# Kernel optimization log

Measured on AMD Instinct MI355X. Metric: run time of the kernel, lower is better.

Reference implementation:

```python
import jax, jax.numpy as jnp
import numpy as np

B, C, D, H, W = 4, 64, 16, 16, 16
C8 = C // 8


def setup_inputs() -> dict:
    key = jax.random.key(0)
    ks = jax.random.split(key, 9)
    s = lambda k, sh: jax.random.normal(k, sh, dtype=jnp.float32)
    return {
        "x_source": s(ks[0], (B, C, D, H, W)),
        "x_target": s(ks[1], (B, C, D, H, W)),
        "Wq": s(ks[2], (C8, C)) * 0.05,
        "bq": s(ks[3], (C8,)) * 0.05,
        "Wk": s(ks[4], (C8, C)) * 0.05,
        "bk": s(ks[5], (C8,)) * 0.05,
        "Wv": s(ks[6], (C, C)) * 0.05,
        "bv": s(ks[7], (C,)) * 0.05,
        "gamma": s(ks[8], (1,)) * 0.1,
    }


def reference(x_source, x_target, Wq, bq, Wk, bk, Wv, bv, gamma):
    b, c, d, h, w = x_source.shape
    n = d * h * w
    xs = x_source.reshape(b, c, n)   # (B, C, N)
    xt = x_target.reshape(b, c, n)
    # 1x1x1 convs == per-token linear projections
    q = jnp.einsum("oc,bcn->bno", Wq, xt) + bq[None, None, :]   # (B, N, C8)
    k = jnp.einsum("oc,bcn->bon", Wk, xs) + bk[None, :, None]   # (B, C8, N)
    v = jnp.einsum("oc,bcn->bon", Wv, xs) + bv[None, :, None]   # (B, C, N)
    # unscaled single-head full attention over all N = D*H*W tokens
    attn = jax.nn.softmax(jnp.einsum("bno,bom->bnm", q, k), axis=-1)  # (B, N, N)
    out = jnp.einsum("bcm,bnm->bcn", v, attn)                   # (B, C, N)
    out = out.reshape(b, c, d, h, w)
    return gamma * out + x_target
```

## Files before the change

### kernel.cpp

```cpp
#include <hip/hip_runtime.h>
#include <hip/hip_bf16.h>


typedef __attribute__((ext_vector_type(8)))  short s16x8;
typedef __attribute__((ext_vector_type(16))) float f32x16;

constexpr int B  = 4;
constexpr int C  = 64;
constexpr int N  = 4096;
constexpr int CH = 32;
constexpr int NC = 32;

__device__ __forceinline__ ushort f2bf(float x) {
    union { __hip_bfloat16 h; ushort u; } cv;
    cv.h = __float2bfloat16(x);
    return cv.u;
}
__device__ __forceinline__ uint pk2(float a, float b) {
    union { __hip_bfloat162 h2; uint u; } cv;
    cv.h2.x = __float2bfloat16(a);
    cv.h2.y = __float2bfloat16(b);
    return cv.u;
}
__device__ __forceinline__ float exp2_fast(float x) {
#if __has_builtin(__builtin_amdgcn_exp2f)
    return __builtin_amdgcn_exp2f(x);
#else
    float e;
    asm("v_exp_f32 %0, %1" : "=v"(e) : "v"(x));
    return e;
#endif
}

__global__ __launch_bounds__(320) void proj_kernel(
    const float* __restrict__ xs, const float* __restrict__ xt,
    const float* __restrict__ Wq, const float* __restrict__ bq,
    const float* __restrict__ Wk, const float* __restrict__ bk,
    const float* __restrict__ Wv, const float* __restrict__ bv,
    ushort* __restrict__ qg, ushort* __restrict__ kg, ushort* __restrict__ vf)
{
    __shared__ float sWv[64 * 64];
    __shared__ float sWk[8 * 64];
    __shared__ float sWq[8 * 64];
    __shared__ float sB[80];

    const int tid = threadIdx.x;
    for (int i = tid; i < 4096; i += 320) sWv[i] = Wv[i];
    for (int i = tid; i < 512;  i += 320) { sWk[i] = Wk[i]; sWq[i] = Wq[i]; }
    if (tid < 64)                sB[tid] = bv[tid];
    else if (tid < 72)           sB[tid] = bk[tid - 64];
    else if (tid < 80)           sB[tid] = bq[tid - 72];
    __syncthreads();

    const int grp = tid >> 5;
    const int tok = tid & 31;
    const int b   = blockIdx.x >> 7;
    const int n   = ((blockIdx.x & 127) << 5) + tok;

    const float* Wsel; const float* bsel; const float* xsel;
    if (grp < 8)       { Wsel = sWv + grp * 8 * C; bsel = sB + grp * 8; xsel = xs; }
    else if (grp == 8) { Wsel = sWk;               bsel = sB + 64;      xsel = xs; }
    else               { Wsel = sWq;               bsel = sB + 72;      xsel = xt; }

    float acc[8];
#pragma unroll
    for (int j = 0; j < 8; j++) acc[j] = bsel[j];

    const float* xcol = xsel + (size_t)b * C * N + n;
#pragma unroll 2
    for (int ci = 0; ci < C; ci += 4) {
        float x0 = xcol[(size_t)(ci + 0) * N];
        float x1 = xcol[(size_t)(ci + 1) * N];
        float x2 = xcol[(size_t)(ci + 2) * N];
        float x3 = xcol[(size_t)(ci + 3) * N];
#pragma unroll
        for (int j = 0; j < 8; j++) {
            const float4 w4 = *(const float4*)&Wsel[j * C + ci];
            acc[j] += w4.x * x0 + w4.y * x1 + w4.z * x2 + w4.w * x3;
        }
    }

    if (grp < 8) {
        const int c   = n >> 5;
        const int kk  = n & 31;
        const int ks  = kk >> 4;
        const int Gd  = (kk >> 3) & 1;
        const int j   = kk & 7;
        const int f   = grp >> 2;
        const int cb  = (grp & 3) * 8;
        ushort* base = vf + ((size_t)(b * 128 + c) * 2048) + ks * 1024 + f * 512 + j;
#pragma unroll
        for (int jc = 0; jc < 8; jc++)
            base[(size_t)(Gd * 32 + cb + jc) * 8] = f2bf(acc[jc]);
    } else {
        if (grp == 9) {
#pragma unroll
            for (int j = 0; j < 8; j++) acc[j] *= 1.4426950408889634f;
        }
        uint4 wv;
        wv.x = pk2(acc[0], acc[1]); wv.y = pk2(acc[2], acc[3]);
        wv.z = pk2(acc[4], acc[5]); wv.w = pk2(acc[6], acc[7]);
        ushort* dst = (grp == 8 ? kg : qg) + ((size_t)b * N + n) * 8;
        *(uint4*)dst = wv;
    }
}

__global__ __launch_bounds__(512, 2) void attn_kernel(
    const ushort* __restrict__ qg, const ushort* __restrict__ kg,
    const ushort* __restrict__ vf, const float* __restrict__ xt,
    const float* __restrict__ gamma, float* __restrict__ out)
{
    __shared__ float comb[2][3][64][33];
    __shared__ float combd[2][3][32];

    const int tid  = threadIdx.x;
    const int w    = tid >> 6;
    const int l    = tid & 63;
    const int q32  = l & 31;
    const int G    = l >> 5;
    const bool g1  = (G != 0);

    const int bid  = blockIdx.x;
    const int xcd  = bid & 7;
    const int slot = bid >> 3;
    const int b    = xcd >> 1;
    const int tp   = ((xcd & 1) << 5) | slot;

    const int tile    = w >> 2;
    const int quarter = w & 3;
    const int qbase   = tp * 64 + tile * 32;
    const int kbase   = quarter * 1024;
    const int cbase   = quarter * 32;

    const ushort* kgb = kg + (size_t)b * N * 8;
    const ushort* qgb = qg + (size_t)b * N * 8;
    const ushort* vfb = vf + (size_t)b * 128 * 2048;

    s16x8 qf;
    {
        const s16x8 z8 = {};
        const s16x8 qv = *(const s16x8*)(qgb + (size_t)(qbase + q32) * 8);
        qf = g1 ? z8 : qv;
    }

    auto kload = [&](int chunk) -> s16x8 {
        return *(const s16x8*)(kgb + (size_t)(kbase + chunk * CH + q32) * 8);
    };
    const ushort* vl = vfb + (size_t)l * 8;

    f32x16 acc0 = {}; f32x16 acc1 = {};
    float d0 = 0.f, d1 = 0.f, d2 = 0.f, d3 = 0.f;

    s16x8 kcur = kload(0);
    s16x8 va0, va1, va2, va3;
    {
        const ushort* vc = vl + (size_t)cbase * 2048;
        va0 = *(const s16x8*)(vc + 0);
        va1 = *(const s16x8*)(vc + 512);
        va2 = *(const s16x8*)(vc + 1024);
        va3 = *(const s16x8*)(vc + 1536);
    }

#pragma unroll 2
    for (int c0 = 0; c0 < NC; ++c0) {
        const int cn  = (c0 + 1 < NC) ? c0 + 1 : c0;
        const s16x8 knx = kload(cn);
        const ushort* vc = vl + (size_t)(cbase + cn) * 2048;
        const s16x8 vb0 = *(const s16x8*)(vc + 0);
        const s16x8 vb1 = *(const s16x8*)(vc + 512);
        const s16x8 vb2 = *(const s16x8*)(vc + 1024);
        const s16x8 vb3 = *(const s16x8*)(vc + 1536);

        __builtin_amdgcn_s_barrier();

        f32x16 sf = {};
        sf = __builtin_amdgcn_mfma_f32_32x32x16_bf16(kcur, qf, sf, 0, 0, 0);

        float p[16];
#pragma unroll
        for (int r = 0; r < 16; r++) p[r] = exp2_fast(sf[r]);
#pragma unroll
        for (int r = 0; r < 16; r += 4) {
            d0 += p[r]; d1 += p[r + 1]; d2 += p[r + 2]; d3 += p[r + 3];
        }

#pragma unroll
        for (int ks = 0; ks < 2; ++ks) {
            uint wd[4];
#pragma unroll
            for (int i = 0; i < 2; i++) {
                const int base = 2 * i + 8 * ks;
                const uint XO = pk2(p[base + 0], p[base + 1]);
                const uint XH = pk2(p[base + 4], p[base + 5]);
                const uint Y  = g1 ? XO : XH;
                const uint Z  = (uint)__shfl_xor((int)Y, 32);
                wd[0 + i] = g1 ? Z : XO;
                wd[2 + i] = g1 ? XH : Z;
            }
            union { uint u[4]; s16x8 v; } bu;
            bu.u[0] = wd[0]; bu.u[1] = wd[1]; bu.u[2] = wd[2]; bu.u[3] = wd[3];

            const s16x8 a0 = ks ? va2 : va0;
            const s16x8 a1 = ks ? va3 : va1;
            acc0 = __builtin_amdgcn_mfma_f32_32x32x16_bf16(a0, bu.v, acc0, 0, 0, 0);
            acc1 = __builtin_amdgcn_mfma_f32_32x32x16_bf16(a1, bu.v, acc1, 0, 0, 0);
        }

        kcur = knx;
        va0 = vb0; va1 = vb1; va2 = vb2; va3 = vb3;
    }

    float dsum = (d0 + d1) + (d2 + d3);
    dsum += __shfl_xor(dsum, 32);

    if (quarter != 0) {
        float* row = &comb[tile][quarter - 1][l][0];
#pragma unroll
        for (int e = 0; e < 16; e++) row[e]      = acc0[e];
#pragma unroll
        for (int e = 0; e < 16; e++) row[16 + e] = acc1[e];
        if (l < 32) combd[tile][quarter - 1][l] = dsum;
    }
    __syncthreads();
    if (quarter == 0) {
        const float g    = gamma[0];
        const float dtot = dsum + combd[tile][0][q32]
                                + combd[tile][1][q32]
                                + combd[tile][2][q32];
        const float inv  = 1.0f / dtot;
        const float* r0  = &comb[tile][0][l][0];
        const float* r1  = &comb[tile][1][l][0];
        const float* r2  = &comb[tile][2][l][0];
#pragma unroll
        for (int r = 0; r < 16; r++) {
            const int crow = (r & 3) + 8 * (r >> 2) + 4 * G;
            const size_t a0 = ((size_t)b * C + crow) * N + qbase + q32;
            const size_t a1 = ((size_t)b * C + crow + 32) * N + qbase + q32;
            const float o0 = (acc0[r] + r0[r]      + r1[r]      + r2[r])      * inv;
            const float o1 = (acc1[r] + r0[16 + r] + r1[16 + r] + r2[16 + r]) * inv;
            out[a0] = g * o0 + xt[a0];
            out[a1] = g * o1 + xt[a1];
        }
    }
}

extern "C" void kernel_launch(void* const* d_in, const int* in_sizes, int n_in,
                              void* d_out, int out_size, void* d_ws, size_t ws_size,
                              hipStream_t stream) {
    const float* xs    = (const float*)d_in[0];
    const float* xt    = (const float*)d_in[1];
    const float* Wq    = (const float*)d_in[2];
    const float* bq    = (const float*)d_in[3];
    const float* Wk    = (const float*)d_in[4];
    const float* bk    = (const float*)d_in[5];
    const float* Wv    = (const float*)d_in[6];
    const float* bv    = (const float*)d_in[7];
    const float* gamma = (const float*)d_in[8];
    float* out = (float*)d_out;

    ushort* qg = (ushort*)d_ws;
    ushort* kg = qg + (size_t)B * N * 8;
    ushort* vfp = kg + (size_t)B * N * 8;

    proj_kernel<<<(B * N) / 32, 320, 0, stream>>>(xs, xt, Wq, bq, Wk, bk, Wv, bv,
                                                  qg, kg, vfp);
    attn_kernel<<<B * 64, 512, 0, stream>>>(qg, kg, vfp, xt, gamma, out);
}
```

Before: 114.0 us.

## Share K/V loads across two query tiles per wave, tree-reduce partials in LDS

The attention kernel now has each wave process both 32-query tiles of a 64-query block over a 512-key slice. Each K and V fragment loaded is reused for two query tiles, halving global K/V traffic per block, and the per-iteration s_barrier is removed. Partial outputs and denominators from the 8 waves are combined by a log-depth LDS tree reduction, and the lane-half exchange uses v_permlane32_swap instead of shuffles. The projection kernel now stages V through LDS so the reordered V layout is written with coalesced 16-byte stores. The cost is higher register pressure from four accumulators and several extra block syncs in the reduction.

```diff
diff --git a/kernel.cpp b/kernel.cpp
--- a/kernel.cpp
+++ b/kernel.cpp
@@ -9,7 +9,7 @@
 constexpr int C  = 64;
 constexpr int N  = 4096;
 constexpr int CH = 32;
-constexpr int NC = 32;
+constexpr int NCW = 16;
 
 __device__ __forceinline__ ushort f2bf(float x) {
     union { __hip_bfloat16 h; ushort u; } cv;
@@ -43,19 +43,21 @@
     __shared__ float sWk[8 * 64];
     __shared__ float sWq[8 * 64];
     __shared__ float sB[80];
+    __shared__ ushort vt[32][68];
 
     const int tid = threadIdx.x;
     for (int i = tid; i < 4096; i += 320) sWv[i] = Wv[i];
     for (int i = tid; i < 512;  i += 320) { sWk[i] = Wk[i]; sWq[i] = Wq[i]; }
-    if (tid < 64)                sB[tid] = bv[tid];
-    else if (tid < 72)           sB[tid] = bk[tid - 64];
-    else if (tid < 80)           sB[tid] = bq[tid - 72];
+    if (tid < 64)       sB[tid] = bv[tid];
+    else if (tid < 72)  sB[tid] = bk[tid - 64];
+    else if (tid < 80)  sB[tid] = bq[tid - 72];
     __syncthreads();
 
     const int grp = tid >> 5;
     const int tok = tid & 31;
     const int b   = blockIdx.x >> 7;
-    const int n   = ((blockIdx.x & 127) << 5) + tok;
+    const int c   = blockIdx.x & 127;
+    const int n   = (c << 5) + tok;
 
     const float* Wsel; const float* bsel; const float* xsel;
     if (grp < 8)       { Wsel = sWv + grp * 8 * C; bsel = sB + grp * 8; xsel = xs; }
@@ -81,17 +83,8 @@
     }
 
     if (grp < 8) {
-        const int c   = n >> 5;
-        const int kk  = n & 31;
-        const int ks  = kk >> 4;
-        const int Gd  = (kk >> 3) & 1;
-        const int j   = kk & 7;
-        const int f   = grp >> 2;
-        const int cb  = (grp & 3) * 8;
-        ushort* base = vf + ((size_t)(b * 128 + c) * 2048) + ks * 1024 + f * 512 + j;
-#pragma unroll
-        for (int jc = 0; jc < 8; jc++)
-            base[(size_t)(Gd * 32 + cb + jc) * 8] = f2bf(acc[jc]);
+#pragma unroll
+        for (int jc = 0; jc < 8; jc++) vt[tok][grp * 8 + jc] = f2bf(acc[jc]);
     } else {
         if (grp == 9) {
 #pragma unroll
@@ -103,6 +96,24 @@
         ushort* dst = (grp == 8 ? kg : qg) + ((size_t)b * N + n) * 8;
         *(uint4*)dst = wv;
     }
+    __syncthreads();
+
+    if (tid < 256) {
+        const int ks = tid >> 7;
+        const int f  = (tid >> 6) & 1;
+        const int ln = tid & 63;
+        const int ch = f * 32 + (ln & 31);
+        const int kkb = ks * 16 + (ln >> 5) * 8;
+        ushort u[8];
+#pragma unroll
+        for (int j = 0; j < 8; j++) u[j] = vt[kkb + j][ch];
+        uint4 wv;
+        wv.x = (uint)u[0] | ((uint)u[1] << 16);
+        wv.y = (uint)u[2] | ((uint)u[3] << 16);
+        wv.z = (uint)u[4] | ((uint)u[5] << 16);
+        wv.w = (uint)u[6] | ((uint)u[7] << 16);
+        *(uint4*)(vf + ((size_t)(b * 128 + c) * 2048) + tid * 8) = wv;
+    }
 }
 
 __global__ __launch_bounds__(512, 2) void attn_kernel(
@@ -110,8 +121,8 @@
     const ushort* __restrict__ vf, const float* __restrict__ xt,
     const float* __restrict__ gamma, float* __restrict__ out)
 {
-    __shared__ float comb[2][3][64][33];
-    __shared__ float combd[2][3][32];
+    __shared__ float cb[4][64][66];
+    __shared__ float cd[4][64];
 
     const int tid  = threadIdx.x;
     const int w    = tid >> 6;
@@ -122,126 +133,153 @@
 
     const int bid  = blockIdx.x;
     const int xcd  = bid & 7;
-    const int slot = bid >> 3;
     const int b    = xcd >> 1;
-    const int tp   = ((xcd & 1) << 5) | slot;
-
-    const int tile    = w >> 2;
-    const int quarter = w & 3;
-    const int qbase   = tp * 64 + tile * 32;
-    const int kbase   = quarter * 1024;
-    const int cbase   = quarter * 32;
+    const int qt   = ((xcd & 1) << 5) | (bid >> 3);
+    const int qbase = qt * 64;
+    const int kbase = w * 512;
 
     const ushort* kgb = kg + (size_t)b * N * 8;
     const ushort* qgb = qg + (size_t)b * N * 8;
     const ushort* vfb = vf + (size_t)b * 128 * 2048;
 
-    s16x8 qf;
+    s16x8 qf0, qf1;
     {
         const s16x8 z8 = {};
-        const s16x8 qv = *(const s16x8*)(qgb + (size_t)(qbase + q32) * 8);
-        qf = g1 ? z8 : qv;
-    }
-
-    auto kload = [&](int chunk) -> s16x8 {
-        return *(const s16x8*)(kgb + (size_t)(kbase + chunk * CH + q32) * 8);
+        const s16x8 qa = *(const s16x8*)(qgb + (size_t)(qbase + q32) * 8);
+        const s16x8 qb = *(const s16x8*)(qgb + (size_t)(qbase + 32 + q32) * 8);
+        qf0 = g1 ? z8 : qa;
+        qf1 = g1 ? z8 : qb;
+    }
+
+    auto kload = [&](int c) -> s16x8 {
+        return *(const s16x8*)(kgb + (size_t)(kbase + c * CH + q32) * 8);
     };
     const ushort* vl = vfb + (size_t)l * 8;
 
-    f32x16 acc0 = {}; f32x16 acc1 = {};
-    float d0 = 0.f, d1 = 0.f, d2 = 0.f, d3 = 0.f;
+    f32x16 acc00 = {}, acc01 = {}, acc10 = {}, acc11 = {};
+    float dn0 = 0.f, dn1 = 0.f;
 
     s16x8 kcur = kload(0);
-    s16x8 va0, va1, va2, va3;
+    s16x8 va00, va01, va10, va11;
     {
-        const ushort* vc = vl + (size_t)cbase * 2048;
-        va0 = *(const s16x8*)(vc + 0);
-        va1 = *(const s16x8*)(vc + 512);
-        va2 = *(const s16x8*)(vc + 1024);
-        va3 = *(const s16x8*)(vc + 1536);
+        const ushort* vc = vl + (size_t)(w * NCW) * 2048;
+        va00 = *(const s16x8*)(vc + 0);
+        va01 = *(const s16x8*)(vc + 512);
+        va10 = *(const s16x8*)(vc + 1024);
+        va11 = *(const s16x8*)(vc + 1536);
     }
 
 #pragma unroll 2
-    for (int c0 = 0; c0 < NC; ++c0) {
-        const int cn  = (c0 + 1 < NC) ? c0 + 1 : c0;
+    for (int c0 = 0; c0 < NCW; ++c0) {
+        const int cn = (c0 + 1 < NCW) ? c0 + 1 : c0;
         const s16x8 knx = kload(cn);
-        const ushort* vc = vl + (size_t)(cbase + cn) * 2048;
-        const s16x8 vb0 = *(const s16x8*)(vc + 0);
-        const s16x8 vb1 = *(const s16x8*)(vc + 512);
-        const s16x8 vb2 = *(const s16x8*)(vc + 1024);
-        const s16x8 vb3 = *(const s16x8*)(vc + 1536);
-
-        __builtin_amdgcn_s_barrier();
-
-        f32x16 sf = {};
-        sf = __builtin_amdgcn_mfma_f32_32x32x16_bf16(kcur, qf, sf, 0, 0, 0);
-
-        float p[16];
-#pragma unroll
-        for (int r = 0; r < 16; r++) p[r] = exp2_fast(sf[r]);
-#pragma unroll
-        for (int r = 0; r < 16; r += 4) {
-            d0 += p[r]; d1 += p[r + 1]; d2 += p[r + 2]; d3 += p[r + 3];
+        const ushort* vc = vl + (size_t)(w * NCW + cn) * 2048;
+        const s16x8 vb00 = *(const s16x8*)(vc + 0);
+        const s16x8 vb01 = *(const s16x8*)(vc + 512);
+        const s16x8 vb10 = *(const s16x8*)(vc + 1024);
+        const s16x8 vb11 = *(const s16x8*)(vc + 1536);
+
+        f32x16 sf0 = {}, sf1 = {};
+        sf0 = __builtin_amdgcn_mfma_f32_32x32x16_bf16(kcur, qf0, sf0, 0, 0, 0);
+        sf1 = __builtin_amdgcn_mfma_f32_32x32x16_bf16(kcur, qf1, sf1, 0, 0, 0);
+
+        float p0[16], p1[16];
+#pragma unroll
+        for (int r = 0; r < 16; r++) p0[r] = exp2_fast(sf0[r]);
+#pragma unroll
+        for (int r = 0; r < 16; r++) p1[r] = exp2_fast(sf1[r]);
+        dn0 += (((p0[0]+p0[1])+(p0[2]+p0[3])) + ((p0[4]+p0[5])+(p0[6]+p0[7])))
+             + (((p0[8]+p0[9])+(p0[10]+p0[11])) + ((p0[12]+p0[13])+(p0[14]+p0[15])));
+        dn1 += (((p1[0]+p1[1])+(p1[2]+p1[3])) + ((p1[4]+p1[5])+(p1[6]+p1[7])))
+             + (((p1[8]+p1[9])+(p1[10]+p1[11])) + ((p1[12]+p1[13])+(p1[14]+p1[15])));
+
+#pragma unroll
+        for (int ks = 0; ks < 2; ++ks) {
+            union { uint u[4]; s16x8 v; } b0, b1;
+#pragma unroll
+            for (int i = 0; i < 2; i++) {
+                uint lo0 = pk2(p0[8 * ks + 2 * i],     p0[8 * ks + 2 * i + 1]);
+                uint hi0 = pk2(p0[8 * ks + 4 + 2 * i], p0[8 * ks + 5 + 2 * i]);
+                asm("v_permlane32_swap_b32 %0, %1" : "+v"(lo0), "+v"(hi0));
+                b0.u[i] = lo0; b0.u[2 + i] = hi0;
+                uint lo1 = pk2(p1[8 * ks + 2 * i],     p1[8 * ks + 2 * i + 1]);
+                uint hi1 = pk2(p1[8 * ks + 4 + 2 * i], p1[8 * ks + 5 + 2 * i]);
+                asm("v_permlane32_swap_b32 %0, %1" : "+v"(lo1), "+v"(hi1));
+                b1.u[i] = lo1; b1.u[2 + i] = hi1;
+            }
+            const s16x8 a0 = ks ? va10 : va00;
+            const s16x8 a1 = ks ? va11 : va01;
+            acc00 = __builtin_amdgcn_mfma_f32_32x32x16_bf16(a0, b0.v, acc00, 0, 0, 0);
+            acc01 = __builtin_amdgcn_mfma_f32_32x32x16_bf16(a1, b0.v, acc01, 0, 0, 0);
+            acc10 = __builtin_amdgcn_mfma_f32_32x32x16_bf16(a0, b1.v, acc10, 0, 0, 0);
+            acc11 = __builtin_amdgcn_mfma_f32_32x32x16_bf16(a1, b1.v, acc11, 0, 0, 0);
         }
 
-#pragma unroll
-        for (int ks = 0; ks < 2; ++ks) {
-            uint wd[4];
-#pragma unroll
-            for (int i = 0; i < 2; i++) {
-                const int base = 2 * i + 8 * ks;
-                const uint XO = pk2(p[base + 0], p[base + 1]);
-                const uint XH = pk2(p[base + 4], p[base + 5]);
-                const uint Y  = g1 ? XO : XH;
-                const uint Z  = (uint)__shfl_xor((int)Y, 32);
-                wd[0 + i] = g1 ? Z : XO;
-                wd[2 + i] = g1 ? XH : Z;
-            }
-            union { uint u[4]; s16x8 v; } bu;
-            bu.u[0] = wd[0]; bu.u[1] = wd[1]; bu.u[2] = wd[2]; bu.u[3] = wd[3];
-
-            const s16x8 a0 = ks ? va2 : va0;
-            const s16x8 a1 = ks ? va3 : va1;
-            acc0 = __builtin_amdgcn_mfma_f32_32x32x16_bf16(a0, bu.v, acc0, 0, 0, 0);
-            acc1 = __builtin_amdgcn_mfma_f32_32x32x16_bf16(a1, bu.v, acc1, 0, 0, 0);
+        kcur = knx;
+        va00 = vb00; va01 = vb01; va10 = vb10; va11 = vb11;
+    }
+
+    dn0 += __shfl_xor(dn0, 32);
+    dn1 += __shfl_xor(dn1, 32);
+
+#define STORE_SLOT(S)                                                          \
+    {                                                                          \
+        float* s0 = &cb[S][0][0];                                              \
+        _Pragma("unroll")                                                      \
+        for (int r = 0; r < 16; r++) {                                         \
+            const int ch = (r & 3) + 8 * (r >> 2) + 4 * G;                     \
+            s0[(ch)      * 66 + q32]      = acc00[r];                          \
+            s0[(ch + 32) * 66 + q32]      = acc01[r];                          \
+            s0[(ch)      * 66 + 32 + q32] = acc10[r];                          \
+            s0[(ch + 32) * 66 + 32 + q32] = acc11[r];                          \
+        }                                                                      \
+        if (!g1) { cd[S][q32] = dn0; cd[S][32 + q32] = dn1; }                  \
+    }
+#define ADD_SLOT(S)                                                            \
+    {                                                                          \
+        const float* s0 = &cb[S][0][0];                                        \
+        _Pragma("unroll")                                                      \
+        for (int r = 0; r < 16; r++) {                                         \
+            const int ch = (r & 3) + 8 * (r >> 2) + 4 * G;                     \
+            acc00[r] += s0[(ch)      * 66 + q32];                              \
+            acc01[r] += s0[(ch + 32) * 66 + q32];                              \
+            acc10[r] += s0[(ch)      * 66 + 32 + q32];                         \
+            acc11[r] += s0[(ch + 32) * 66 + 32 + q32];                         \
+        }                                                                      \
+        dn0 += cd[S][q32];                                                     \
+        dn1 += cd[S][32 + q32];                                                \
+    }
+
+    if (w >= 4) STORE_SLOT(w - 4);
+    __syncthreads();
+    if (w < 4) ADD_SLOT(w);
+    __syncthreads();
+    if (w == 2 || w == 3) STORE_SLOT(w - 2);
+    __syncthreads();
+    if (w < 2) ADD_SLOT(w);
+    __syncthreads();
+    if (w == 1) STORE_SLOT(0);
+    __syncthreads();
+    if (w == 0) {
+        ADD_SLOT(0);
+        const float g    = gamma[0];
+        const float inv0 = 1.0f / dn0;
+        const float inv1 = 1.0f / dn1;
+#pragma unroll
+        for (int r = 0; r < 16; r++) {
+            const int ch = (r & 3) + 8 * (r >> 2) + 4 * G;
+            const size_t a00 = ((size_t)b * C + ch)      * N + qbase + q32;
+            const size_t a01 = ((size_t)b * C + ch + 32) * N + qbase + q32;
+            const size_t a10 = a00 + 32;
+            const size_t a11 = a01 + 32;
+            out[a00] = g * (acc00[r] * inv0) + xt[a00];
+            out[a01] = g * (acc01[r] * inv0) + xt[a01];
+            out[a10] = g * (acc10[r] * inv1) + xt[a10];
+            out[a11] = g * (acc11[r] * inv1) + xt[a11];
         }
-
-        kcur = knx;
-        va0 = vb0; va1 = vb1; va2 = vb2; va3 = vb3;
-    }
-
-    float dsum = (d0 + d1) + (d2 + d3);
-    dsum += __shfl_xor(dsum, 32);
-
-    if (quarter != 0) {
-        float* row = &comb[tile][quarter - 1][l][0];
-#pragma unroll
-        for (int e = 0; e < 16; e++) row[e]      = acc0[e];
-#pragma unroll
-        for (int e = 0; e < 16; e++) row[16 + e] = acc1[e];
-        if (l < 32) combd[tile][quarter - 1][l] = dsum;
-    }
-    __syncthreads();
-    if (quarter == 0) {
-        const float g    = gamma[0];
-        const float dtot = dsum + combd[tile][0][q32]
-                                + combd[tile][1][q32]
-                                + combd[tile][2][q32];
-        const float inv  = 1.0f / dtot;
-        const float* r0  = &comb[tile][0][l][0];
-        const float* r1  = &comb[tile][1][l][0];
-        const float* r2  = &comb[tile][2][l][0];
-#pragma unroll
-        for (int r = 0; r < 16; r++) {
-            const int crow = (r & 3) + 8 * (r >> 2) + 4 * G;
-            const size_t a0 = ((size_t)b * C + crow) * N + qbase + q32;
-            const size_t a1 = ((size_t)b * C + crow + 32) * N + qbase + q32;
-            const float o0 = (acc0[r] + r0[r]      + r1[r]      + r2[r])      * inv;
-            const float o1 = (acc1[r] + r0[16 + r] + r1[16 + r] + r2[16 + r]) * inv;
-            out[a0] = g * o0 + xt[a0];
-            out[a1] = g * o1 + xt[a1];
-        }
-    }
+    }
+#undef STORE_SLOT
+#undef ADD_SLOT
 }
 
 extern "C" void kernel_launch(void* const* d_in, const int* in_sizes, int n_in,
@@ -258,8 +296,8 @@
     const float* gamma = (const float*)d_in[8];
     float* out = (float*)d_out;
 
-    ushort* qg = (ushort*)d_ws;
-    ushort* kg = qg + (size_t)B * N * 8;
+    ushort* qg  = (ushort*)d_ws;
+    ushort* kg  = qg + (size_t)B * N * 8;
     ushort* vfp = kg + (size_t)B * N * 8;
 
     proj_kernel<<<(B * N) / 32, 320, 0, stream>>>(xs, xt, Wq, bq, Wk, bk, Wv, bv,
```

Result: faster. 110.7 us (-2.8%).
